# Optimization experiments

Measured on AMD Instinct MI355X. Metric: run time of the kernel, lower is better.

The kernel has to match this reference:

```python
import jax, jax.numpy as jnp
import numpy as np
from jax import lax

# --- constants matching init_kwargs ---
NUM_SCALES = 3
LAMBDA_0, MU_0 = 1.0, 0.5
KAPPA_LAMBDA, KAPPA_MU = 2.0, 1.0
BASE_WEIGHT, GRADIENT_SCALING = 1.0, 5.0
CLAMP_MIN, CLAMP_MAX = 0.1, 10.0
SCALE_WEIGHTS = [1.0, 0.5, 0.25]
JAC_PENALTY_W = 0.1
BLUR_KSIZE, BLUR_SIGMA = 5, 1.1  # torchvision default sigma for ksize=5: 0.3*((5-1)*0.5-1)+0.8


def _resize1d_align_corners(x, axis, out_size):
    """Linear resize along one axis with align_corners=True (separable trilinear)."""
    n = x.shape[axis]
    if out_size == n:
        return x
    coords = jnp.arange(out_size, dtype=jnp.float32) * ((n - 1) / max(out_size - 1, 1))
    i0 = jnp.floor(coords).astype(jnp.int32)
    i1 = jnp.minimum(i0 + 1, n - 1)
    w = (coords - i0.astype(jnp.float32)).astype(x.dtype)
    shape = [1] * x.ndim
    shape[axis] = out_size
    w = w.reshape(shape)
    x0 = jnp.take(x, i0, axis=axis)
    x1 = jnp.take(x, i1, axis=axis)
    return x0 * (1 - w) + x1 * w


def trilinear_resize(x, out_sizes):
    # x: (B, C, X, Y, Z); align_corners=True trilinear is separable
    for ax, s in zip((-3, -2, -1), out_sizes):
        x = _resize1d_align_corners(x, ax % x.ndim, s)
    return x


def _blur_axis(x, axis, k):
    r = (BLUR_KSIZE - 1) // 2
    pad = [(0, 0)] * x.ndim
    pad[axis] = (r, r)
    xp = jnp.pad(x, pad, mode='reflect')
    n = x.shape[axis]
    out = jnp.zeros_like(x)
    for t in range(BLUR_KSIZE):
        out = out + k[t] * lax.slice_in_dim(xp, t, t + n, axis=axis)
    return out


def gaussian_blur3d(x):
    t = jnp.arange(BLUR_KSIZE, dtype=jnp.float32) - (BLUR_KSIZE - 1) / 2
    k = jnp.exp(-(t ** 2) / (2.0 * BLUR_SIGMA ** 2))
    k = (k / k.sum()).astype(x.dtype)
    for ax in (-3, -2, -1):
        x = _blur_axis(x, ax % x.ndim, k)
    return x


def jacobian_penalty(deform):
    # 3x3 Jacobian of the displacement at the center voxel via central differences
    B, _, X, Y, Z = deform.shape
    c = (X // 2, Y // 2, Z // 2)
    dx = 0.5 * (deform[:, :, c[0] + 1, c[1], c[2]] - deform[:, :, c[0] - 1, c[1], c[2]])
    dy = 0.5 * (deform[:, :, c[0], c[1] + 1, c[2]] - deform[:, :, c[0], c[1] - 1, c[2]])
    dz = 0.5 * (deform[:, :, c[0], c[1], c[2] + 1] - deform[:, :, c[0], c[1], c[2] - 1])
    J = jnp.stack([dx, dy, dz], axis=-1)  # (B, 3, 3)
    det = jnp.linalg.det(J)
    return jnp.mean(jax.nn.relu(-det))


def _loss_fwd(deformation_field, image):
    B, _, X, Y, Z = deformation_field.shape
    total = jnp.zeros((), dtype=deformation_field.dtype)
    for i in range(NUM_SCALES):
        scale = 2 ** i
        out_sizes = (X // scale, Y // scale, Z // scale)
        deform_s = trilinear_resize(deformation_field, out_sizes)
        image_s = trilinear_resize(image, out_sizes)
        img = image_s[:, 0]  # (B, x, y, z)
        gx, gy, gz = jnp.gradient(img, axis=(-3, -2, -1))
        image_gradient = jnp.sqrt(gx ** 2 + gy ** 2 + gz ** 2)
        ig_sm = gaussian_blur3d(image_gradient[None])  # (1, B, x, y, z)
        lam = jnp.clip(LAMBDA_0 + KAPPA_LAMBDA * ig_sm, CLAMP_MIN, CLAMP_MAX)
        mu = jnp.clip(MU_0 + KAPPA_MU * ig_sm, CLAMP_MIN, CLAMP_MAX)
        du = jnp.gradient(deform_s[:, 0], axis=(-3, -2, -1))
        dv = jnp.gradient(deform_s[:, 1], axis=(-3, -2, -1))
        dw = jnp.gradient(deform_s[:, 2], axis=(-3, -2, -1))
        E_xx, E_yy, E_zz = du[0], dv[1], dw[2]
        E_xy = 0.5 * (du[1] + dv[0])
        E_xz = 0.5 * (du[2] + dw[0])
        E_yz = 0.5 * (dv[2] + dw[1])
        trace_E = E_xx + E_yy + E_zz
        energy = (0.5 * lam * trace_E ** 2
                  + mu * (E_xx ** 2 + E_yy ** 2 + E_zz ** 2
                          + 2.0 * (E_xy ** 2 + E_xz ** 2 + E_yz ** 2)))
        weight = BASE_WEIGHT + GRADIENT_SCALING * ig_sm
        total = total + SCALE_WEIGHTS[i] * jnp.mean(weight * energy)
    total = total + JAC_PENALTY_W * jacobian_penalty(deformation_field)
    return total


def setup_inputs() -> dict:
    key = jax.random.key(0)
    k1, k2 = jax.random.split(key)
    deformation_field = jax.random.normal(k1, (2, 3, 160, 160, 160), dtype=jnp.float32)
    image = jax.random.uniform(k2, (2, 1, 160, 160, 160), dtype=jnp.float32)
    return {"deformation_field": deformation_field, "image": image}


def reference(deformation_field, image):
    return _loss_fwd(deformation_field, image)
```

## Files before the change

kernel.cpp:

```cpp
#include <hip/hip_runtime.h>

#define TPB 256
#define RED_NB 2048

#define K0 0.0707663f
#define K1 0.2444606f
#define K2 0.3695462f

typedef float f4 __attribute__((ext_vector_type(4)));

__device__ __forceinline__ f4 ld4(const float* __restrict__ p) { return *(const f4*)p; }

__device__ __forceinline__ int rref(int i, int n) {
    return i < 0 ? -i : (i >= n ? 2 * n - 2 - i : i);
}

template <int NIN, int M>
__device__ __forceinline__ void resize_one(const float* __restrict__ in,
                                           float* __restrict__ out, long idx) {
    constexpr float ratio = (float)((NIN - 1.0) / (M - 1.0));
    int z = (int)(idx % M); long r = idx / M;
    int y = (int)(r % M);   r /= M;
    int x = (int)(r % M);   int bc = (int)(r / M);

    float cx = (float)x * ratio, cy = (float)y * ratio, cz = (float)z * ratio;
    int x0 = min((int)cx, NIN - 1), y0 = min((int)cy, NIN - 1), z0 = min((int)cz, NIN - 1);
    float wx = cx - (float)x0, wy = cy - (float)y0, wz = cz - (float)z0;
    int x1 = min(x0 + 1, NIN - 1), y1 = min(y0 + 1, NIN - 1), z1 = min(z0 + 1, NIN - 1);

    const float* p = in + (long)bc * NIN * NIN * NIN;
    constexpr long sx = (long)NIN * NIN;
#define AT(xi, yi, zi) p[(long)(xi) * sx + (long)(yi) * NIN + (zi)]
    float c00 = AT(x0, y0, z0) * (1.f - wz) + AT(x0, y0, z1) * wz;
    float c01 = AT(x0, y1, z0) * (1.f - wz) + AT(x0, y1, z1) * wz;
    float c10 = AT(x1, y0, z0) * (1.f - wz) + AT(x1, y0, z1) * wz;
    float c11 = AT(x1, y1, z0) * (1.f - wz) + AT(x1, y1, z1) * wz;
#undef AT
    float c0 = c00 * (1.f - wy) + c01 * wy;
    float c1 = c10 * (1.f - wy) + c11 * wy;
    out[idx] = c0 * (1.f - wx) + c1 * wx;
}

__global__ void resize_all_kernel(const float* __restrict__ D, const float* __restrict__ I,
                                  float* __restrict__ ds1, float* __restrict__ ds2,
                                  float* __restrict__ is1, float* __restrict__ is2,
                                  long A, long Bn, long C, long Dn) {
    long idx = (long)blockIdx.x * blockDim.x + threadIdx.x;
    if (idx < A) { resize_one<160, 80>(D, ds1, idx); return; }
    idx -= A;
    if (idx < Bn) { resize_one<160, 40>(D, ds2, idx); return; }
    idx -= Bn;
    if (idx < C) { resize_one<160, 80>(I, is1, idx); return; }
    idx -= C;
    if (idx < Dn) { resize_one<160, 40>(I, is2, idx); }
}

template <int N>
__global__ void gradmag_v4(const float* __restrict__ img, float* __restrict__ g, int B) {
    constexpr int NZ4 = N / 4;
    constexpr long n2 = (long)N * N, n3 = n2 * N;
    long total = (long)B * N * N * NZ4;
    long idx = (long)blockIdx.x * blockDim.x + threadIdx.x;
    if (idx >= total) return;
    int z4 = (int)(idx % NZ4); long r = idx / NZ4;
    int y = (int)(r % N); r /= N;
    int x = (int)(r % N); int b = (int)(r / N);
    int z = z4 * 4;

    const float* base = img + (long)b * n3;
    const float* rowc = base + (long)x * n2 + (long)y * N;
    f4 cur = ld4(rowc + z);
    f4 prev = (z > 0) ? ld4(rowc + z - 4) : cur;
    f4 next = (z + 4 < N) ? ld4(rowc + z + 4) : cur;

    int xm = max(x - 1, 0), xp = min(x + 1, N - 1);
    int ym = max(y - 1, 0), yp = min(y + 1, N - 1);
    float hx = (x == 0 || x == N - 1) ? 1.f : 0.5f;
    float hy = (y == 0 || y == N - 1) ? 1.f : 0.5f;
    f4 rxp = ld4(base + (long)xp * n2 + (long)y * N + z);
    f4 rxm = ld4(base + (long)xm * n2 + (long)y * N + z);
    f4 ryp = ld4(base + (long)x * n2 + (long)yp * N + z);
    f4 rym = ld4(base + (long)x * n2 + (long)ym * N + z);

    f4 outv;
#pragma unroll
    for (int j = 0; j < 4; ++j) {
        float c = cur[j];
        float zmv = (j == 0) ? prev[3] : cur[(j == 0) ? 0 : j - 1];
        float zpv = (j == 3) ? next[0] : cur[(j == 3) ? 3 : j + 1];
        int gz = z + j;
        float dz = (gz == 0) ? (zpv - c) : ((gz == N - 1) ? (c - zmv) : 0.5f * (zpv - zmv));
        float dx = hx * (rxp[j] - rxm[j]);
        float dy = hy * (ryp[j] - rym[j]);
        outv[j] = sqrtf(dx * dx + dy * dy + dz * dz);
    }
    *(f4*)(g + (long)b * n3 + (long)x * n2 + (long)y * N + z) = outv;
}

template <int N>
__global__ void blur_xy_fused_v4(const float* __restrict__ in, float* __restrict__ out, int B) {
    constexpr int NZ4 = N / 4;
    constexpr long n2 = (long)N * N, n3 = n2 * N;
    long total = (long)B * N * N * NZ4;
    long idx = (long)blockIdx.x * blockDim.x + threadIdx.x;
    if (idx >= total) return;
    int z4 = (int)(idx % NZ4); long r = idx / NZ4;
    int y = (int)(r % N); r /= N;
    int x = (int)(r % N); int b = (int)(r / N);
    int z = z4 * 4;

    const float K[5] = {K0, K1, K2, K1, K0};
    const float* base = in + (long)b * n3;
    f4 acc = {0.f, 0.f, 0.f, 0.f};
#pragma unroll
    for (int i = 0; i < 5; ++i) {
        int qx = rref(x + i - 2, N);
        const float* px = base + (long)qx * n2 + z;
        f4 t = {0.f, 0.f, 0.f, 0.f};
#pragma unroll
        for (int j = 0; j < 5; ++j) {
            int qy = rref(y + j - 2, N);
            t += K[j] * ld4(px + (long)qy * N);
        }
        acc += K[i] * t;
    }
    *(f4*)(out + (long)b * n3 + (long)x * n2 + (long)y * N + z) = acc;
}

template <int N>
__global__ void energy_v4(const float* __restrict__ def, const float* __restrict__ igxy,
                          float* __restrict__ partial, int B) {
    constexpr int NZ4 = N / 4;
    constexpr long n2 = (long)N * N, n3 = n2 * N;
    long total = (long)B * N * N * NZ4;
    float lsum = 0.f;
    for (long idx = (long)blockIdx.x * blockDim.x + threadIdx.x; idx < total;
         idx += (long)gridDim.x * blockDim.x) {
        int z4 = (int)(idx % NZ4); long r = idx / NZ4;
        int y = (int)(r % N); r /= N;
        int x = (int)(r % N); int b = (int)(r / N);
        int z = z4 * 4;

        int xm = max(x - 1, 0), xp = min(x + 1, N - 1);
        int ym = max(y - 1, 0), yp = min(y + 1, N - 1);
        float hx = (x == 0 || x == N - 1) ? 1.f : 0.5f;
        float hy = (y == 0 || y == N - 1) ? 1.f : 0.5f;

        const float* base = def + (long)b * 3 * n3;
        long sp = (long)x * n2 + (long)y * N + z;

        f4 CC[3], CP[3], CN[3], RXP[3], RXM[3], RYP[3], RYM[3];
#pragma unroll
        for (int c = 0; c < 3; ++c) {
            const float* rc = base + (long)c * n3 + sp;
            CC[c] = ld4(rc);
            CP[c] = (z > 0) ? ld4(rc - 4) : CC[c];
            CN[c] = (z + 4 < N) ? ld4(rc + 4) : CC[c];
            RXP[c] = ld4(base + (long)c * n3 + (long)xp * n2 + (long)y * N + z);
            RXM[c] = ld4(base + (long)c * n3 + (long)xm * n2 + (long)y * N + z);
            RYP[c] = ld4(base + (long)c * n3 + (long)x * n2 + (long)yp * N + z);
            RYM[c] = ld4(base + (long)c * n3 + (long)x * n2 + (long)ym * N + z);
        }

        const float* growc = igxy + (long)b * n3 + (long)x * n2 + (long)y * N;
        f4 gcur = ld4(growc + z);
        f4 gprev, gnext;
        if (z >= 4) gprev = ld4(growc + z - 4);
        else { gprev[0] = growc[4]; gprev[1] = growc[3]; gprev[2] = growc[2]; gprev[3] = growc[1]; }
        if (z + 8 <= N) gnext = ld4(growc + z + 4);
        else { gnext[0] = growc[N - 2]; gnext[1] = growc[N - 3]; gnext[2] = growc[N - 4]; gnext[3] = growc[N - 5]; }
        float gw[12];
#pragma unroll
        for (int i = 0; i < 4; ++i) { gw[i] = gprev[i]; gw[4 + i] = gcur[i]; gw[8 + i] = gnext[i]; }

#pragma unroll
        for (int j = 0; j < 4; ++j) {
            int gz = z + j;
            float dX[3], dY[3], dZ[3];
#pragma unroll
            for (int c = 0; c < 3; ++c) {
                float cc = CC[c][j];
                float zmv = (j == 0) ? CP[c][3] : CC[c][(j == 0) ? 0 : j - 1];
                float zpv = (j == 3) ? CN[c][0] : CC[c][(j == 3) ? 3 : j + 1];
                dZ[c] = (gz == 0) ? (zpv - cc)
                                  : ((gz == N - 1) ? (cc - zmv) : 0.5f * (zpv - zmv));
                dX[c] = hx * (RXP[c][j] - RXM[c][j]);
                dY[c] = hy * (RYP[c][j] - RYM[c][j]);
            }
            float igv = K0 * gw[2 + j] + K1 * gw[3 + j] + K2 * gw[4 + j]
                      + K1 * gw[5 + j] + K0 * gw[6 + j];
            float lam = fminf(fmaxf(1.0f + 2.0f * igv, 0.1f), 10.0f);
            float mu  = fminf(fmaxf(0.5f + 1.0f * igv, 0.1f), 10.0f);
            float wt  = 1.0f + 5.0f * igv;

            float Exx = dX[0], Eyy = dY[1], Ezz = dZ[2];
            float Exy = 0.5f * (dY[0] + dX[1]);
            float Exz = 0.5f * (dZ[0] + dX[2]);
            float Eyz = 0.5f * (dZ[1] + dY[2]);
            float tr = Exx + Eyy + Ezz;
            float e = 0.5f * lam * tr * tr +
                      mu * (Exx * Exx + Eyy * Eyy + Ezz * Ezz +
                            2.0f * (Exy * Exy + Exz * Exz + Eyz * Eyz));
            lsum += wt * e;
        }
    }
    __shared__ float sm[TPB];
    sm[threadIdx.x] = lsum;
    __syncthreads();
    for (int s = TPB / 2; s > 0; s >>= 1) {
        if (threadIdx.x < s) sm[threadIdx.x] += sm[threadIdx.x + s];
        __syncthreads();
    }
    if (threadIdx.x == 0) partial[blockIdx.x] = sm[0];
}

__global__ void finalize_kernel(const float* __restrict__ partial,
                                const float* __restrict__ def, float* __restrict__ out) {
    __shared__ float sm[TPB];
    const float wts[3] = {1.0f, 0.5f, 0.25f};
    const float invcnt[3] = {1.0f / (2.0f * 160 * 160 * 160),
                             1.0f / (2.0f * 80 * 80 * 80),
                             1.0f / (2.0f * 40 * 40 * 40)};
    float acc = 0.f;
    for (int s = 0; s < 3; ++s) {
        float local = 0.f;
        for (int i = threadIdx.x; i < RED_NB; i += TPB) local += partial[s * RED_NB + i];
        acc += wts[s] * invcnt[s] * local;
    }
    sm[threadIdx.x] = acc;
    __syncthreads();
    for (int s = TPB / 2; s > 0; s >>= 1) {
        if (threadIdx.x < s) sm[threadIdx.x] += sm[threadIdx.x + s];
        __syncthreads();
    }
    if (threadIdx.x == 0) {
        float jac = 0.f;
        const int n = 160;
        long n3 = (long)n * n * n;
        long ctr = ((long)80 * n + 80) * n + 80;
        for (int b = 0; b < 2; ++b) {
            const float* p = def + (long)b * 3 * n3;
            float J[3][3];
            for (int c = 0; c < 3; ++c) {
                const float* q = p + (long)c * n3 + ctr;
                J[c][0] = 0.5f * (q[(long)n * n] - q[-(long)n * n]);
                J[c][1] = 0.5f * (q[n] - q[-n]);
                J[c][2] = 0.5f * (q[1] - q[-1]);
            }
            float det = J[0][0] * (J[1][1] * J[2][2] - J[1][2] * J[2][1])
                      - J[0][1] * (J[1][0] * J[2][2] - J[1][2] * J[2][0])
                      + J[0][2] * (J[1][0] * J[2][1] - J[1][1] * J[2][0]);
            jac += fmaxf(-det, 0.f);
        }
        jac *= 0.5f;
        out[0] = sm[0] + 0.1f * jac;
    }
}

extern "C" void kernel_launch(void* const* d_in, const int* in_sizes, int n_in,
                              void* d_out, int out_size, void* d_ws, size_t ws_size,
                              hipStream_t stream) {
    const float* D = (const float*)d_in[0];
    const float* I = (const float*)d_in[1];
    float* out = (float*)d_out;
    float* ws = (float*)d_ws;

    const int B = 2;
    const long S0 = (long)B * 160 * 160 * 160;
    const long S1 = (long)B * 80 * 80 * 80;
    const long S2 = (long)B * 40 * 40 * 40;

    float* partials = ws;
    float* ds1 = partials + 3 * RED_NB;
    float* is1 = ds1 + 3 * S1;
    float* g1  = is1 + S1;
    float* t1  = g1 + S1;
    float* ds2 = t1 + S1;
    float* is2 = ds2 + 3 * S2;
    float* g2  = is2 + S2;
    float* t2  = g2 + S2;
    float* g0  = t2 + S2;
    float* t0  = g0 + S0;

    {
        long A = 3 * S1, Bn = 3 * S2, C = S1, Dn = S2;
        long tot = A + Bn + C + Dn;
        resize_all_kernel<<<(int)((tot + TPB - 1) / TPB), TPB, 0, stream>>>(
            D, I, ds1, ds2, is1, is2, A, Bn, C, Dn);
    }

    {
        long total4 = S0 / 4;
        int blocks = (int)((total4 + TPB - 1) / TPB);
        gradmag_v4<160><<<blocks, TPB, 0, stream>>>(I, g0, B);
        blur_xy_fused_v4<160><<<blocks, TPB, 0, stream>>>(g0, t0, B);
        energy_v4<160><<<RED_NB, TPB, 0, stream>>>(D, t0, partials + 0 * RED_NB, B);
    }

    {
        long total4 = S1 / 4;
        int blocks = (int)((total4 + TPB - 1) / TPB);
        gradmag_v4<80><<<blocks, TPB, 0, stream>>>(is1, g1, B);
        blur_xy_fused_v4<80><<<blocks, TPB, 0, stream>>>(g1, t1, B);
        energy_v4<80><<<RED_NB, TPB, 0, stream>>>(ds1, t1, partials + 1 * RED_NB, B);
    }

    {
        long total4 = S2 / 4;
        int blocks = (int)((total4 + TPB - 1) / TPB);
        gradmag_v4<40><<<blocks, TPB, 0, stream>>>(is2, g2, B);
        blur_xy_fused_v4<40><<<blocks, TPB, 0, stream>>>(g2, t2, B);
        energy_v4<40><<<RED_NB, TPB, 0, stream>>>(ds2, t2, partials + 2 * RED_NB, B);
    }

    finalize_kernel<<<1, TPB, 0, stream>>>(partials, D, out);
}
```

Before: 171.0 us.

## Register-block blur over 4 y rows and walk z chunks in energy kernel

After: 236.8 us. 38.4% more time.

```diff
diff --git a/kernel.cpp b/kernel.cpp
--- a/kernel.cpp
+++ b/kernel.cpp
@@ -41,10 +41,11 @@
     out[idx] = c0 * (1.f - wx) + c1 * wx;
 }
 
-__global__ void resize_all_kernel(const float* __restrict__ D, const float* __restrict__ I,
-                                  float* __restrict__ ds1, float* __restrict__ ds2,
-                                  float* __restrict__ is1, float* __restrict__ is2,
-                                  long A, long Bn, long C, long Dn) {
+__global__ __launch_bounds__(TPB)
+void resize_all_kernel(const float* __restrict__ D, const float* __restrict__ I,
+                       float* __restrict__ ds1, float* __restrict__ ds2,
+                       float* __restrict__ is1, float* __restrict__ is2,
+                       long A, long Bn, long C, long Dn) {
     long idx = (long)blockIdx.x * blockDim.x + threadIdx.x;
     if (idx < A) { resize_one<160, 80>(D, ds1, idx); return; }
     idx -= A;
@@ -56,7 +57,8 @@
 }
 
 template <int N>
-__global__ void gradmag_v4(const float* __restrict__ img, float* __restrict__ g, int B) {
+__global__ __launch_bounds__(TPB)
+void gradmag_v4(const float* __restrict__ img, float* __restrict__ g, int B) {
     constexpr int NZ4 = N / 4;
     constexpr long n2 = (long)N * N, n3 = n2 * N;
     long total = (long)B * N * N * NZ4;
@@ -98,80 +100,95 @@
 }
 
 template <int N>
-__global__ void blur_xy_fused_v4(const float* __restrict__ in, float* __restrict__ out, int B) {
-    constexpr int NZ4 = N / 4;
+__global__ __launch_bounds__(TPB)
+void blur_xy_y4(const float* __restrict__ in, float* __restrict__ out, int B) {
+    constexpr int NZ4 = N / 4, NY4 = N / 4;
     constexpr long n2 = (long)N * N, n3 = n2 * N;
-    long total = (long)B * N * N * NZ4;
+    long total = (long)B * N * NY4 * NZ4;
     long idx = (long)blockIdx.x * blockDim.x + threadIdx.x;
     if (idx >= total) return;
     int z4 = (int)(idx % NZ4); long r = idx / NZ4;
+    int y4 = (int)(r % NY4); r /= NY4;
+    int x = (int)(r % N); int b = (int)(r / N);
+    int y0 = y4 * 4, z = z4 * 4;
+
+    const float K[5] = {K0, K1, K2, K1, K0};
+    const float* base = in + (long)b * n3 + z;
+
+    f4 cs[8];
+#pragma unroll
+    for (int jj = 0; jj < 8; ++jj) cs[jj] = (f4){0.f, 0.f, 0.f, 0.f};
+
+#pragma unroll
+    for (int i = 0; i < 5; ++i) {
+        int qx = rref(x + i - 2, N);
+        const float* px = base + (long)qx * n2;
+#pragma unroll
+        for (int jj = 0; jj < 8; ++jj) {
+            int qy = rref(y0 - 2 + jj, N);
+            cs[jj] += K[i] * ld4(px + (long)qy * N);
+        }
+    }
+    float* ob = out + (long)b * n3 + (long)x * n2 + z;
+#pragma unroll
+    for (int k = 0; k < 4; ++k) {
+        f4 o = K0 * cs[k] + K1 * cs[k + 1] + K2 * cs[k + 2] + K1 * cs[k + 3] + K0 * cs[k + 4];
+        *(f4*)(ob + (long)(y0 + k) * N) = o;
+    }
+}
+
+template <int N, int ZC4, int NCH>
+__global__ __launch_bounds__(TPB)
+void energy_walk(const float* __restrict__ def, const float* __restrict__ igxy,
+                 float* __restrict__ partial, int B) {
+    constexpr long n2 = (long)N * N, n3 = n2 * N;
+    long idx = (long)blockIdx.x * blockDim.x + threadIdx.x;
+    int chk = (int)(idx % NCH); long r = idx / NCH;
     int y = (int)(r % N); r /= N;
     int x = (int)(r % N); int b = (int)(r / N);
-    int z = z4 * 4;
-
-    const float K[5] = {K0, K1, K2, K1, K0};
-    const float* base = in + (long)b * n3;
-    f4 acc = {0.f, 0.f, 0.f, 0.f};
-#pragma unroll
-    for (int i = 0; i < 5; ++i) {
-        int qx = rref(x + i - 2, N);
-        const float* px = base + (long)qx * n2 + z;
-        f4 t = {0.f, 0.f, 0.f, 0.f};
-#pragma unroll
-        for (int j = 0; j < 5; ++j) {
-            int qy = rref(y + j - 2, N);
-            t += K[j] * ld4(px + (long)qy * N);
-        }
-        acc += K[i] * t;
-    }
-    *(f4*)(out + (long)b * n3 + (long)x * n2 + (long)y * N + z) = acc;
-}
-
-template <int N>
-__global__ void energy_v4(const float* __restrict__ def, const float* __restrict__ igxy,
-                          float* __restrict__ partial, int B) {
-    constexpr int NZ4 = N / 4;
-    constexpr long n2 = (long)N * N, n3 = n2 * N;
-    long total = (long)B * N * N * NZ4;
+    int z0 = chk * ZC4 * 4;
+
+    int xm = max(x - 1, 0), xp = min(x + 1, N - 1);
+    int ym = max(y - 1, 0), yp = min(y + 1, N - 1);
+    float hx = (x == 0 || x == N - 1) ? 1.f : 0.5f;
+    float hy = (y == 0 || y == N - 1) ? 1.f : 0.5f;
+
+    const float* base = def + (long)b * 3 * n3;
+    const float* rc0 = base + (long)x * n2 + (long)y * N;
+    long oxp = (long)(xp - x) * n2, oxm = (long)(xm - x) * n2;
+    long oyp = (long)(yp - y) * N,  oym = (long)(ym - y) * N;
+    const float* grow = igxy + (long)b * n3 + (long)x * n2 + (long)y * N;
+
+    f4 P[3], C[3], Nx[3];
+#pragma unroll
+    for (int c = 0; c < 3; ++c) {
+        const float* rc = rc0 + (long)c * n3;
+        C[c] = ld4(rc + z0);
+        P[c] = (z0 > 0) ? ld4(rc + z0 - 4) : C[c];
+    }
+    f4 gc = ld4(grow + z0);
+    f4 gn = ld4(grow + z0 + 4);
+    f4 gp;
+    if (z0 >= 4) gp = ld4(grow + z0 - 4);
+    else { gp[0] = gn[0]; gp[1] = gc[3]; gp[2] = gc[2]; gp[3] = gc[1]; }
+
     float lsum = 0.f;
-    for (long idx = (long)blockIdx.x * blockDim.x + threadIdx.x; idx < total;
-         idx += (long)gridDim.x * blockDim.x) {
-        int z4 = (int)(idx % NZ4); long r = idx / NZ4;
-        int y = (int)(r % N); r /= N;
-        int x = (int)(r % N); int b = (int)(r / N);
-        int z = z4 * 4;
-
-        int xm = max(x - 1, 0), xp = min(x + 1, N - 1);
-        int ym = max(y - 1, 0), yp = min(y + 1, N - 1);
-        float hx = (x == 0 || x == N - 1) ? 1.f : 0.5f;
-        float hy = (y == 0 || y == N - 1) ? 1.f : 0.5f;
-
-        const float* base = def + (long)b * 3 * n3;
-        long sp = (long)x * n2 + (long)y * N + z;
-
-        f4 CC[3], CP[3], CN[3], RXP[3], RXM[3], RYP[3], RYM[3];
+#pragma unroll
+    for (int k = 0; k < ZC4; ++k) {
+        int z = z0 + 4 * k;
+        f4 RXP[3], RXM[3], RYP[3], RYM[3];
 #pragma unroll
         for (int c = 0; c < 3; ++c) {
-            const float* rc = base + (long)c * n3 + sp;
-            CC[c] = ld4(rc);
-            CP[c] = (z > 0) ? ld4(rc - 4) : CC[c];
-            CN[c] = (z + 4 < N) ? ld4(rc + 4) : CC[c];
-            RXP[c] = ld4(base + (long)c * n3 + (long)xp * n2 + (long)y * N + z);
-            RXM[c] = ld4(base + (long)c * n3 + (long)xm * n2 + (long)y * N + z);
-            RYP[c] = ld4(base + (long)c * n3 + (long)x * n2 + (long)yp * N + z);
-            RYM[c] = ld4(base + (long)c * n3 + (long)x * n2 + (long)ym * N + z);
-        }
-
-        const float* growc = igxy + (long)b * n3 + (long)x * n2 + (long)y * N;
-        f4 gcur = ld4(growc + z);
-        f4 gprev, gnext;
-        if (z >= 4) gprev = ld4(growc + z - 4);
-        else { gprev[0] = growc[4]; gprev[1] = growc[3]; gprev[2] = growc[2]; gprev[3] = growc[1]; }
-        if (z + 8 <= N) gnext = ld4(growc + z + 4);
-        else { gnext[0] = growc[N - 2]; gnext[1] = growc[N - 3]; gnext[2] = growc[N - 4]; gnext[3] = growc[N - 5]; }
+            const float* rc = rc0 + (long)c * n3 + z;
+            Nx[c] = (z + 8 <= N) ? ld4(rc + 4) : C[c];
+            RXP[c] = ld4(rc + oxp);
+            RXM[c] = ld4(rc + oxm);
+            RYP[c] = ld4(rc + oyp);
+            RYM[c] = ld4(rc + oym);
+        }
         float gw[12];
 #pragma unroll
-        for (int i = 0; i < 4; ++i) { gw[i] = gprev[i]; gw[4 + i] = gcur[i]; gw[8 + i] = gnext[i]; }
+        for (int i = 0; i < 4; ++i) { gw[i] = gp[i]; gw[4 + i] = gc[i]; gw[8 + i] = gn[i]; }
 
 #pragma unroll
         for (int j = 0; j < 4; ++j) {
@@ -179,9 +196,9 @@
             float dX[3], dY[3], dZ[3];
 #pragma unroll
             for (int c = 0; c < 3; ++c) {
-                float cc = CC[c][j];
-                float zmv = (j == 0) ? CP[c][3] : CC[c][(j == 0) ? 0 : j - 1];
-                float zpv = (j == 3) ? CN[c][0] : CC[c][(j == 3) ? 3 : j + 1];
+                float cc = C[c][j];
+                float zmv = (j == 0) ? P[c][3] : C[c][(j == 0) ? 0 : j - 1];
+                float zpv = (j == 3) ? Nx[c][0] : C[c][(j == 3) ? 3 : j + 1];
                 dZ[c] = (gz == 0) ? (zpv - cc)
                                   : ((gz == N - 1) ? (cc - zmv) : 0.5f * (zpv - zmv));
                 dX[c] = hx * (RXP[c][j] - RXM[c][j]);
@@ -203,7 +220,17 @@
                             2.0f * (Exy * Exy + Exz * Exz + Eyz * Eyz));
             lsum += wt * e;
         }
-    }
+
+        if (k + 1 < ZC4) {
+#pragma unroll
+            for (int c = 0; c < 3; ++c) { P[c] = C[c]; C[c] = Nx[c]; }
+            f4 ngp = gc, ngc = gn, ngn;
+            if (z + 12 <= N) ngn = ld4(grow + z + 8);
+            else { ngn[0] = ngc[2]; ngn[1] = ngc[1]; ngn[2] = ngc[0]; ngn[3] = ngp[3]; }
+            gp = ngp; gc = ngc; gn = ngn;
+        }
+    }
+
     __shared__ float sm[TPB];
     sm[threadIdx.x] = lsum;
     __syncthreads();
@@ -214,17 +241,20 @@
     if (threadIdx.x == 0) partial[blockIdx.x] = sm[0];
 }
 
-__global__ void finalize_kernel(const float* __restrict__ partial,
-                                const float* __restrict__ def, float* __restrict__ out) {
+__global__ __launch_bounds__(TPB)
+void finalize_kernel(const float* __restrict__ partial,
+                     const float* __restrict__ def, float* __restrict__ out) {
     __shared__ float sm[TPB];
     const float wts[3] = {1.0f, 0.5f, 0.25f};
     const float invcnt[3] = {1.0f / (2.0f * 160 * 160 * 160),
                              1.0f / (2.0f * 80 * 80 * 80),
                              1.0f / (2.0f * 40 * 40 * 40)};
+    const int offs[3] = {0, 1600, 1800};
+    const int cnts[3] = {1600, 200, 25};
     float acc = 0.f;
     for (int s = 0; s < 3; ++s) {
         float local = 0.f;
-        for (int i = threadIdx.x; i < RED_NB; i += TPB) local += partial[s * RED_NB + i];
+        for (int i = threadIdx.x; i < cnts[s]; i += TPB) local += partial[offs[s] + i];
         acc += wts[s] * invcnt[s] * local;
     }
     sm[threadIdx.x] = acc;
@@ -293,24 +323,27 @@
         long total4 = S0 / 4;
         int blocks = (int)((total4 + TPB - 1) / TPB);
         gradmag_v4<160><<<blocks, TPB, 0, stream>>>(I, g0, B);
-        blur_xy_fused_v4<160><<<blocks, TPB, 0, stream>>>(g0, t0, B);
-        energy_v4<160><<<RED_NB, TPB, 0, stream>>>(D, t0, partials + 0 * RED_NB, B);
+        long btot = (long)B * 160 * 40 * 40;
+        blur_xy_y4<160><<<(int)((btot + TPB - 1) / TPB), TPB, 0, stream>>>(g0, t0, B);
+        energy_walk<160, 5, 8><<<1600, TPB, 0, stream>>>(D, t0, partials + 0, B);
     }
 
     {
         long total4 = S1 / 4;
         int blocks = (int)((total4 + TPB - 1) / TPB);
         gradmag_v4<80><<<blocks, TPB, 0, stream>>>(is1, g1, B);
-        blur_xy_fused_v4<80><<<blocks, TPB, 0, stream>>>(g1, t1, B);
-        energy_v4<80><<<RED_NB, TPB, 0, stream>>>(ds1, t1, partials + 1 * RED_NB, B);
+        long btot = (long)B * 80 * 20 * 20;
+        blur_xy_y4<80><<<(int)((btot + TPB - 1) / TPB), TPB, 0, stream>>>(g1, t1, B);
+        energy_walk<80, 5, 4><<<200, TPB, 0, stream>>>(ds1, t1, partials + 1600, B);
     }
 
     {
         long total4 = S2 / 4;
         int blocks = (int)((total4 + TPB - 1) / TPB);
         gradmag_v4<40><<<blocks, TPB, 0, stream>>>(is2, g2, B);
-        blur_xy_fused_v4<40><<<blocks, TPB, 0, stream>>>(g2, t2, B);
-        energy_v4<40><<<RED_NB, TPB, 0, stream>>>(ds2, t2, partials + 2 * RED_NB, B);
+        long btot = (long)B * 40 * 10 * 10;
+        blur_xy_y4<40><<<(int)((btot + TPB - 1) / TPB), TPB, 0, stream>>>(g2, t2, B);
+        energy_walk<40, 5, 2><<<25, TPB, 0, stream>>>(ds2, t2, partials + 1800, B);
     }
 
     finalize_kernel<<<1, TPB, 0, stream>>>(partials, D, out);
```

## Merge per-scale kernels into single launches and register-block the XY blur

Applied to the files above, without the earlier changes.

Result: faster. 163.7 us (-4.3%).

```diff
diff --git a/kernel.cpp b/kernel.cpp
--- a/kernel.cpp
+++ b/kernel.cpp
@@ -1,11 +1,17 @@
 #include <hip/hip_runtime.h>
 
 #define TPB 256
-#define RED_NB 2048
 
 #define K0 0.0707663f
 #define K1 0.2444606f
 #define K2 0.3695462f
+
+#define EB0 8000
+#define EB1 1000
+#define EB2 125
+#define BB0 2000
+#define BB1 250
+#define BB2 32
 
 typedef float f4 __attribute__((ext_vector_type(4)));
 
@@ -41,10 +47,11 @@
     out[idx] = c0 * (1.f - wx) + c1 * wx;
 }
 
-__global__ void resize_all_kernel(const float* __restrict__ D, const float* __restrict__ I,
-                                  float* __restrict__ ds1, float* __restrict__ ds2,
-                                  float* __restrict__ is1, float* __restrict__ is2,
-                                  long A, long Bn, long C, long Dn) {
+__global__ __launch_bounds__(TPB)
+void resize_all_kernel(const float* __restrict__ D, const float* __restrict__ I,
+                       float* __restrict__ ds1, float* __restrict__ ds2,
+                       float* __restrict__ is1, float* __restrict__ is2,
+                       long A, long Bn, long C, long Dn) {
     long idx = (long)blockIdx.x * blockDim.x + threadIdx.x;
     if (idx < A) { resize_one<160, 80>(D, ds1, idx); return; }
     idx -= A;
@@ -56,12 +63,10 @@
 }
 
 template <int N>
-__global__ void gradmag_v4(const float* __restrict__ img, float* __restrict__ g, int B) {
+__device__ __forceinline__ void gradmag_one(const float* __restrict__ img,
+                                            float* __restrict__ g, long idx) {
     constexpr int NZ4 = N / 4;
     constexpr long n2 = (long)N * N, n3 = n2 * N;
-    long total = (long)B * N * N * NZ4;
-    long idx = (long)blockIdx.x * blockDim.x + threadIdx.x;
-    if (idx >= total) return;
     int z4 = (int)(idx % NZ4); long r = idx / NZ4;
     int y = (int)(r % N); r /= N;
     int x = (int)(r % N); int b = (int)(r / N);
@@ -97,113 +102,151 @@
     *(f4*)(g + (long)b * n3 + (long)x * n2 + (long)y * N + z) = outv;
 }
 
+__global__ __launch_bounds__(TPB)
+void gradmag_all(const float* __restrict__ I0, const float* __restrict__ is1,
+                 const float* __restrict__ is2, float* __restrict__ g0,
+                 float* __restrict__ g1, float* __restrict__ g2) {
+    int blk = blockIdx.x;
+    if (blk < EB0)            gradmag_one<160>(I0,  g0, (long)blk * TPB + threadIdx.x);
+    else if (blk < EB0 + EB1) gradmag_one<80> (is1, g1, (long)(blk - EB0) * TPB + threadIdx.x);
+    else                      gradmag_one<40> (is2, g2, (long)(blk - EB0 - EB1) * TPB + threadIdx.x);
+}
+
 template <int N>
-__global__ void blur_xy_fused_v4(const float* __restrict__ in, float* __restrict__ out, int B) {
+__device__ __forceinline__ void blur_one(const float* __restrict__ in,
+                                         float* __restrict__ out, long idx) {
+    constexpr int NZ4 = N / 4, NY4 = N / 4;
+    constexpr long n2 = (long)N * N, n3 = n2 * N;
+    int z4 = (int)(idx % NZ4); long r = idx / NZ4;
+    int y4 = (int)(r % NY4); r /= NY4;
+    int x = (int)(r % N); int b = (int)(r / N);
+    int y0 = y4 * 4, z = z4 * 4;
+
+    const float K[5] = {K0, K1, K2, K1, K0};
+    const float* base = in + (long)b * n3 + z;
+
+    f4 cs[8];
+#pragma unroll
+    for (int jj = 0; jj < 8; ++jj) cs[jj] = (f4){0.f, 0.f, 0.f, 0.f};
+
+#pragma unroll
+    for (int i = 0; i < 5; ++i) {
+        int qx = rref(x + i - 2, N);
+        const float* px = base + (long)qx * n2;
+#pragma unroll
+        for (int jj = 0; jj < 8; ++jj) {
+            int qy = rref(y0 - 2 + jj, N);
+            cs[jj] += K[i] * ld4(px + (long)qy * N);
+        }
+    }
+    float* ob = out + (long)b * n3 + (long)x * n2 + z;
+#pragma unroll
+    for (int k = 0; k < 4; ++k) {
+        f4 o = K0 * cs[k] + K1 * cs[k + 1] + K2 * cs[k + 2] + K1 * cs[k + 3] + K0 * cs[k + 4];
+        *(f4*)(ob + (long)(y0 + k) * N) = o;
+    }
+}
+
+__global__ __launch_bounds__(TPB)
+void blur_all(const float* __restrict__ g0, const float* __restrict__ g1,
+              const float* __restrict__ g2, float* __restrict__ t0,
+              float* __restrict__ t1, float* __restrict__ t2) {
+    int blk = blockIdx.x;
+    if (blk < BB0)            blur_one<160>(g0, t0, (long)blk * TPB + threadIdx.x);
+    else if (blk < BB0 + BB1) blur_one<80> (g1, t1, (long)(blk - BB0) * TPB + threadIdx.x);
+    else {
+        long idx = (long)(blk - BB0 - BB1) * TPB + threadIdx.x;
+        if (idx < (long)2 * 40 * 10 * 10) blur_one<40>(g2, t2, idx);
+    }
+}
+
+template <int N>
+__device__ __forceinline__ float energy_one(const float* __restrict__ def,
+                                            const float* __restrict__ igxy, long idx) {
     constexpr int NZ4 = N / 4;
     constexpr long n2 = (long)N * N, n3 = n2 * N;
-    long total = (long)B * N * N * NZ4;
-    long idx = (long)blockIdx.x * blockDim.x + threadIdx.x;
-    if (idx >= total) return;
     int z4 = (int)(idx % NZ4); long r = idx / NZ4;
     int y = (int)(r % N); r /= N;
     int x = (int)(r % N); int b = (int)(r / N);
     int z = z4 * 4;
 
-    const float K[5] = {K0, K1, K2, K1, K0};
-    const float* base = in + (long)b * n3;
-    f4 acc = {0.f, 0.f, 0.f, 0.f};
-#pragma unroll
-    for (int i = 0; i < 5; ++i) {
-        int qx = rref(x + i - 2, N);
-        const float* px = base + (long)qx * n2 + z;
-        f4 t = {0.f, 0.f, 0.f, 0.f};
-#pragma unroll
-        for (int j = 0; j < 5; ++j) {
-            int qy = rref(y + j - 2, N);
-            t += K[j] * ld4(px + (long)qy * N);
+    int xm = max(x - 1, 0), xp = min(x + 1, N - 1);
+    int ym = max(y - 1, 0), yp = min(y + 1, N - 1);
+    float hx = (x == 0 || x == N - 1) ? 1.f : 0.5f;
+    float hy = (y == 0 || y == N - 1) ? 1.f : 0.5f;
+
+    const float* base = def + (long)b * 3 * n3;
+    long sp = (long)x * n2 + (long)y * N + z;
+
+    f4 CC[3], CP[3], CN[3], RXP[3], RXM[3], RYP[3], RYM[3];
+#pragma unroll
+    for (int c = 0; c < 3; ++c) {
+        const float* rc = base + (long)c * n3 + sp;
+        CC[c] = ld4(rc);
+        CP[c] = (z > 0) ? ld4(rc - 4) : CC[c];
+        CN[c] = (z + 4 < N) ? ld4(rc + 4) : CC[c];
+        RXP[c] = ld4(base + (long)c * n3 + (long)xp * n2 + (long)y * N + z);
+        RXM[c] = ld4(base + (long)c * n3 + (long)xm * n2 + (long)y * N + z);
+        RYP[c] = ld4(base + (long)c * n3 + (long)x * n2 + (long)yp * N + z);
+        RYM[c] = ld4(base + (long)c * n3 + (long)x * n2 + (long)ym * N + z);
+    }
+
+    const float* growc = igxy + (long)b * n3 + (long)x * n2 + (long)y * N;
+    f4 gcur = ld4(growc + z);
+    f4 gprev, gnext;
+    if (z >= 4) gprev = ld4(growc + z - 4);
+    else { gprev[0] = growc[4]; gprev[1] = growc[3]; gprev[2] = growc[2]; gprev[3] = growc[1]; }
+    if (z + 8 <= N) gnext = ld4(growc + z + 4);
+    else { gnext[0] = growc[N - 2]; gnext[1] = growc[N - 3]; gnext[2] = growc[N - 4]; gnext[3] = growc[N - 5]; }
+    float gw[12];
+#pragma unroll
+    for (int i = 0; i < 4; ++i) { gw[i] = gprev[i]; gw[4 + i] = gcur[i]; gw[8 + i] = gnext[i]; }
+
+    float lsum = 0.f;
+#pragma unroll
+    for (int j = 0; j < 4; ++j) {
+        int gz = z + j;
+        float dX[3], dY[3], dZ[3];
+#pragma unroll
+        for (int c = 0; c < 3; ++c) {
+            float cc = CC[c][j];
+            float zmv = (j == 0) ? CP[c][3] : CC[c][(j == 0) ? 0 : j - 1];
+            float zpv = (j == 3) ? CN[c][0] : CC[c][(j == 3) ? 3 : j + 1];
+            dZ[c] = (gz == 0) ? (zpv - cc)
+                              : ((gz == N - 1) ? (cc - zmv) : 0.5f * (zpv - zmv));
+            dX[c] = hx * (RXP[c][j] - RXM[c][j]);
+            dY[c] = hy * (RYP[c][j] - RYM[c][j]);
         }
-        acc += K[i] * t;
-    }
-    *(f4*)(out + (long)b * n3 + (long)x * n2 + (long)y * N + z) = acc;
-}
-
-template <int N>
-__global__ void energy_v4(const float* __restrict__ def, const float* __restrict__ igxy,
-                          float* __restrict__ partial, int B) {
-    constexpr int NZ4 = N / 4;
-    constexpr long n2 = (long)N * N, n3 = n2 * N;
-    long total = (long)B * N * N * NZ4;
-    float lsum = 0.f;
-    for (long idx = (long)blockIdx.x * blockDim.x + threadIdx.x; idx < total;
-         idx += (long)gridDim.x * blockDim.x) {
-        int z4 = (int)(idx % NZ4); long r = idx / NZ4;
-        int y = (int)(r % N); r /= N;
-        int x = (int)(r % N); int b = (int)(r / N);
-        int z = z4 * 4;
-
-        int xm = max(x - 1, 0), xp = min(x + 1, N - 1);
-        int ym = max(y - 1, 0), yp = min(y + 1, N - 1);
-        float hx = (x == 0 || x == N - 1) ? 1.f : 0.5f;
-        float hy = (y == 0 || y == N - 1) ? 1.f : 0.5f;
-
-        const float* base = def + (long)b * 3 * n3;
-        long sp = (long)x * n2 + (long)y * N + z;
-
-        f4 CC[3], CP[3], CN[3], RXP[3], RXM[3], RYP[3], RYM[3];
-#pragma unroll
-        for (int c = 0; c < 3; ++c) {
-            const float* rc = base + (long)c * n3 + sp;
-            CC[c] = ld4(rc);
-            CP[c] = (z > 0) ? ld4(rc - 4) : CC[c];
-            CN[c] = (z + 4 < N) ? ld4(rc + 4) : CC[c];
-            RXP[c] = ld4(base + (long)c * n3 + (long)xp * n2 + (long)y * N + z);
-            RXM[c] = ld4(base + (long)c * n3 + (long)xm * n2 + (long)y * N + z);
-            RYP[c] = ld4(base + (long)c * n3 + (long)x * n2 + (long)yp * N + z);
-            RYM[c] = ld4(base + (long)c * n3 + (long)x * n2 + (long)ym * N + z);
-        }
-
-        const float* growc = igxy + (long)b * n3 + (long)x * n2 + (long)y * N;
-        f4 gcur = ld4(growc + z);
-        f4 gprev, gnext;
-        if (z >= 4) gprev = ld4(growc + z - 4);
-        else { gprev[0] = growc[4]; gprev[1] = growc[3]; gprev[2] = growc[2]; gprev[3] = growc[1]; }
-        if (z + 8 <= N) gnext = ld4(growc + z + 4);
-        else { gnext[0] = growc[N - 2]; gnext[1] = growc[N - 3]; gnext[2] = growc[N - 4]; gnext[3] = growc[N - 5]; }
-        float gw[12];
-#pragma unroll
-        for (int i = 0; i < 4; ++i) { gw[i] = gprev[i]; gw[4 + i] = gcur[i]; gw[8 + i] = gnext[i]; }
-
-#pragma unroll
-        for (int j = 0; j < 4; ++j) {
-            int gz = z + j;
-            float dX[3], dY[3], dZ[3];
-#pragma unroll
-            for (int c = 0; c < 3; ++c) {
-                float cc = CC[c][j];
-                float zmv = (j == 0) ? CP[c][3] : CC[c][(j == 0) ? 0 : j - 1];
-                float zpv = (j == 3) ? CN[c][0] : CC[c][(j == 3) ? 3 : j + 1];
-                dZ[c] = (gz == 0) ? (zpv - cc)
-                                  : ((gz == N - 1) ? (cc - zmv) : 0.5f * (zpv - zmv));
-                dX[c] = hx * (RXP[c][j] - RXM[c][j]);
-                dY[c] = hy * (RYP[c][j] - RYM[c][j]);
-            }
-            float igv = K0 * gw[2 + j] + K1 * gw[3 + j] + K2 * gw[4 + j]
-                      + K1 * gw[5 + j] + K0 * gw[6 + j];
-            float lam = fminf(fmaxf(1.0f + 2.0f * igv, 0.1f), 10.0f);
-            float mu  = fminf(fmaxf(0.5f + 1.0f * igv, 0.1f), 10.0f);
-            float wt  = 1.0f + 5.0f * igv;
-
-            float Exx = dX[0], Eyy = dY[1], Ezz = dZ[2];
-            float Exy = 0.5f * (dY[0] + dX[1]);
-            float Exz = 0.5f * (dZ[0] + dX[2]);
-            float Eyz = 0.5f * (dZ[1] + dY[2]);
-            float tr = Exx + Eyy + Ezz;
-            float e = 0.5f * lam * tr * tr +
-                      mu * (Exx * Exx + Eyy * Eyy + Ezz * Ezz +
-                            2.0f * (Exy * Exy + Exz * Exz + Eyz * Eyz));
-            lsum += wt * e;
-        }
-    }
+        float igv = K0 * gw[2 + j] + K1 * gw[3 + j] + K2 * gw[4 + j]
+                  + K1 * gw[5 + j] + K0 * gw[6 + j];
+        float lam = fminf(fmaxf(1.0f + 2.0f * igv, 0.1f), 10.0f);
+        float mu  = fminf(fmaxf(0.5f + 1.0f * igv, 0.1f), 10.0f);
+        float wt  = 1.0f + 5.0f * igv;
+
+        float Exx = dX[0], Eyy = dY[1], Ezz = dZ[2];
+        float Exy = 0.5f * (dY[0] + dX[1]);
+        float Exz = 0.5f * (dZ[0] + dX[2]);
+        float Eyz = 0.5f * (dZ[1] + dY[2]);
+        float tr = Exx + Eyy + Ezz;
+        float e = 0.5f * lam * tr * tr +
+                  mu * (Exx * Exx + Eyy * Eyy + Ezz * Ezz +
+                        2.0f * (Exy * Exy + Exz * Exz + Eyz * Eyz));
+        lsum += wt * e;
+    }
+    return lsum;
+}
+
+__global__ __launch_bounds__(TPB)
+void energy_all(const float* __restrict__ D, const float* __restrict__ ds1,
+                const float* __restrict__ ds2, const float* __restrict__ t0,
+                const float* __restrict__ t1, const float* __restrict__ t2,
+                float* __restrict__ partial) {
+    int blk = blockIdx.x;
+    float lsum;
+    if (blk < EB0)            lsum = energy_one<160>(D,   t0, (long)blk * TPB + threadIdx.x);
+    else if (blk < EB0 + EB1) lsum = energy_one<80> (ds1, t1, (long)(blk - EB0) * TPB + threadIdx.x);
+    else                      lsum = energy_one<40> (ds2, t2, (long)(blk - EB0 - EB1) * TPB + threadIdx.x);
+
     __shared__ float sm[TPB];
     sm[threadIdx.x] = lsum;
     __syncthreads();
@@ -211,20 +254,23 @@
         if (threadIdx.x < s) sm[threadIdx.x] += sm[threadIdx.x + s];
         __syncthreads();
     }
-    if (threadIdx.x == 0) partial[blockIdx.x] = sm[0];
-}
-
-__global__ void finalize_kernel(const float* __restrict__ partial,
-                                const float* __restrict__ def, float* __restrict__ out) {
+    if (threadIdx.x == 0) partial[blk] = sm[0];
+}
+
+__global__ __launch_bounds__(TPB)
+void finalize_kernel(const float* __restrict__ partial,
+                     const float* __restrict__ def, float* __restrict__ out) {
     __shared__ float sm[TPB];
     const float wts[3] = {1.0f, 0.5f, 0.25f};
     const float invcnt[3] = {1.0f / (2.0f * 160 * 160 * 160),
                              1.0f / (2.0f * 80 * 80 * 80),
                              1.0f / (2.0f * 40 * 40 * 40)};
+    const int offs[3] = {0, EB0, EB0 + EB1};
+    const int cnts[3] = {EB0, EB1, EB2};
     float acc = 0.f;
     for (int s = 0; s < 3; ++s) {
         float local = 0.f;
-        for (int i = threadIdx.x; i < RED_NB; i += TPB) local += partial[s * RED_NB + i];
+        for (int i = threadIdx.x; i < cnts[s]; i += TPB) local += partial[offs[s] + i];
         acc += wts[s] * invcnt[s] * local;
     }
     sm[threadIdx.x] = acc;
@@ -271,7 +317,7 @@
     const long S2 = (long)B * 40 * 40 * 40;
 
     float* partials = ws;
-    float* ds1 = partials + 3 * RED_NB;
+    float* ds1 = partials + 9216;
     float* is1 = ds1 + 3 * S1;
     float* g1  = is1 + S1;
     float* t1  = g1 + S1;
@@ -288,30 +334,8 @@
         resize_all_kernel<<<(int)((tot + TPB - 1) / TPB), TPB, 0, stream>>>(
             D, I, ds1, ds2, is1, is2, A, Bn, C, Dn);
     }
-
-    {
-        long total4 = S0 / 4;
-        int blocks = (int)((total4 + TPB - 1) / TPB);
-        gradmag_v4<160><<<blocks, TPB, 0, stream>>>(I, g0, B);
-        blur_xy_fused_v4<160><<<blocks, TPB, 0, stream>>>(g0, t0, B);
-        energy_v4<160><<<RED_NB, TPB, 0, stream>>>(D, t0, partials + 0 * RED_NB, B);
-    }
-
-    {
-        long total4 = S1 / 4;
-        int blocks = (int)((total4 + TPB - 1) / TPB);
-        gradmag_v4<80><<<blocks, TPB, 0, stream>>>(is1, g1, B);
-        blur_xy_fused_v4<80><<<blocks, TPB, 0, stream>>>(g1, t1, B);
-        energy_v4<80><<<RED_NB, TPB, 0, stream>>>(ds1, t1, partials + 1 * RED_NB, B);
-    }
-
-    {
-        long total4 = S2 / 4;
-        int blocks = (int)((total4 + TPB - 1) / TPB);
-        gradmag_v4<40><<<blocks, TPB, 0, stream>>>(is2, g2, B);
-        blur_xy_fused_v4<40><<<blocks, TPB, 0, stream>>>(g2, t2, B);
-        energy_v4<40><<<RED_NB, TPB, 0, stream>>>(ds2, t2, partials + 2 * RED_NB, B);
-    }
-
+    gradmag_all<<<EB0 + EB1 + EB2, TPB, 0, stream>>>(I, is1, is2, g0, g1, g2);
+    blur_all<<<BB0 + BB1 + BB2, TPB, 0, stream>>>(g0, g1, g2, t0, t1, t2);
+    energy_all<<<EB0 + EB1 + EB2, TPB, 0, stream>>>(D, ds1, ds2, t0, t1, t2, partials);
     finalize_kernel<<<1, TPB, 0, stream>>>(partials, D, out);
 }
```
